# Optimization experiments

Measured on AMD Instinct MI355X. Metric: run time of the kernel, lower is better.

The kernel has to match this reference:

```python
import jax, jax.numpy as jnp
import numpy as np

NUM_HEADS = 16
DIM_HEAD = 64
SCALE = DIM_HEAD ** -0.5
ROPE_BASE = 10000.0


def _rope(t):
    # t: [b, h, n, d] -> rotary embedding with rotate-half convention
    n, d = t.shape[2], t.shape[3]
    inv_freq = 1.0 / (ROPE_BASE ** (jnp.arange(0, d, 2, dtype=jnp.float32) / d))
    freqs = jnp.arange(n, dtype=jnp.float32)[:, None] * inv_freq[None, :]  # [n, d/2]
    cos = jnp.concatenate([jnp.cos(freqs), jnp.cos(freqs)], axis=-1)  # [n, d]
    sin = jnp.concatenate([jnp.sin(freqs), jnp.sin(freqs)], axis=-1)
    t1, t2 = jnp.split(t, 2, axis=-1)
    rot = jnp.concatenate([-t2, t1], axis=-1)
    return t * cos + rot * sin


def setup_inputs() -> dict:
    key = jax.random.key(0)
    k1, k2, k3 = jax.random.split(key, 3)
    B, N, D = 2, 2049, 1024  # 2048 patches + 1 cls token
    x = jax.random.normal(k1, (B, N, D), dtype=jnp.float32)
    ln_gamma = jnp.ones((D,), dtype=jnp.float32)
    ln_beta = jnp.zeros((D,), dtype=jnp.float32)
    w_qkv = jax.random.normal(k2, (D, 3 * NUM_HEADS * DIM_HEAD), dtype=jnp.float32) * 0.02
    w_out = jax.random.normal(k3, (NUM_HEADS * DIM_HEAD, D), dtype=jnp.float32) * 0.02
    return {"x": x, "ln_gamma": ln_gamma, "ln_beta": ln_beta, "w_qkv": w_qkv, "w_out": w_out}


def reference(x, ln_gamma, ln_beta, w_qkv, w_out):
    B, N, D = x.shape
    # LayerNorm (eps=1e-5, torch default)
    mu = jnp.mean(x, axis=-1, keepdims=True)
    var = jnp.mean(jnp.square(x - mu), axis=-1, keepdims=True)
    xn = (x - mu) * jax.lax.rsqrt(var + 1e-5) * ln_gamma + ln_beta
    # QKV projection (no bias)
    qkv = xn @ w_qkv  # [B, N, 3*H*Dh]
    q, k, v = jnp.split(qkv, 3, axis=-1)
    def to_heads(t):
        return t.reshape(B, N, NUM_HEADS, DIM_HEAD).transpose(0, 2, 1, 3)  # [B,H,N,Dh]
    q, k, v = to_heads(q), to_heads(k), to_heads(v)
    # cls token excluded from RoPE
    q = jnp.concatenate([q[:, :, :1, :], _rope(q[:, :, 1:, :])], axis=2)
    k = jnp.concatenate([k[:, :, :1, :], _rope(k[:, :, 1:, :])], axis=2)
    dots = jnp.einsum('bhqd,bhkd->bhqk', q, k) * SCALE
    attn = jax.nn.softmax(dots, axis=-1)
    out = jnp.einsum('bhqk,bhkd->bhqd', attn, v)
    out = out.transpose(0, 2, 1, 3).reshape(B, N, NUM_HEADS * DIM_HEAD)
    return out @ w_out
```

## Files before the change

kernel.cpp:

```cpp
#include <hip/hip_runtime.h>

#define B_    2
#define N_    2049
#define NPAD  2112
#define D_    1024
#define H_    16
#define DH    64
#define MROWS (B_ * N_)
#define MPAD  4224
#define QSCALE 0.18033688011117674f

using bf16x8 = __attribute__((ext_vector_type(8))) short;
using f32x4  = __attribute__((ext_vector_type(4))) float;
using f32x16 = __attribute__((ext_vector_type(16))) float;

#define AS1 __attribute__((address_space(1)))
#define AS3 __attribute__((address_space(3)))

__device__ __forceinline__ float bf2f(short s) {
  union { unsigned u; float f; } a; a.u = ((unsigned)(unsigned short)s) << 16; return a.f;
}
__device__ __forceinline__ short f2bf(float f) {
  union { float f; unsigned u; } a; a.f = f;
  unsigned r = a.u + 0x7fffu + ((a.u >> 16) & 1u);
  return (short)(r >> 16);
}
__device__ __forceinline__ unsigned pack_trunc(float lo, float hi) {
  union { float f; unsigned u; } a, b; a.f = lo; b.f = hi;
  return (b.u & 0xffff0000u) | (a.u >> 16);
}
__device__ __forceinline__ float hexp2(float x) { return __builtin_amdgcn_exp2f(x); }
__device__ __forceinline__ void dma16(const short* g, AS3 short* l) {
  __builtin_amdgcn_global_load_lds((const AS1 unsigned*)g, (AS3 unsigned*)l, 16, 0, 0);
}

__global__ __launch_bounds__(256) void ln_kernel(const float* __restrict__ x,
                                                 const float* __restrict__ gamma,
                                                 const float* __restrict__ beta,
                                                 short* __restrict__ xn) {
  int row = blockIdx.x;
  int tid = threadIdx.x;
  const float4 v = ((const float4*)(x + (size_t)row * D_))[tid];
  float s  = v.x + v.y + v.z + v.w;
  float ss = v.x * v.x + v.y * v.y + v.z * v.z + v.w * v.w;
  for (int o = 1; o < 64; o <<= 1) { s += __shfl_xor(s, o, 64); ss += __shfl_xor(ss, o, 64); }
  __shared__ float sb[4], s2b[4];
  int wid = tid >> 6;
  if ((tid & 63) == 0) { sb[wid] = s; s2b[wid] = ss; }
  __syncthreads();
  float st  = sb[0] + sb[1] + sb[2] + sb[3];
  float sst = s2b[0] + s2b[1] + s2b[2] + s2b[3];
  float mu  = st * (1.0f / D_);
  float var = sst * (1.0f / D_) - mu * mu;
  float rs  = rsqrtf(var + 1e-5f);
  const float4 g  = ((const float4*)gamma)[tid];
  const float4 be = ((const float4*)beta)[tid];
  short4 o4;
  o4.x = f2bf((v.x - mu) * rs * g.x + be.x);
  o4.y = f2bf((v.y - mu) * rs * g.y + be.y);
  o4.z = f2bf((v.z - mu) * rs * g.z + be.z);
  o4.w = f2bf((v.w - mu) * rs * g.w + be.w);
  ((short4*)(xn + (size_t)row * D_))[tid] = o4;
}

__global__ __launch_bounds__(256) void transpose_tiled(const float* __restrict__ in,
                                                       short* __restrict__ out,
                                                       int K, int Nn) {
  __shared__ float T[64][65];
  int k0 = blockIdx.x * 64;
  int n0 = blockIdx.y * 64;
  int t = threadIdx.x;
  int r = t >> 2, c0 = (t & 3) * 16;
  const float* ip = in + (size_t)(k0 + r) * Nn + n0 + c0;
  #pragma unroll
  for (int j = 0; j < 4; ++j) {
    float4 v = *(const float4*)(ip + j * 4);
    T[r][c0 + j * 4 + 0] = v.x; T[r][c0 + j * 4 + 1] = v.y;
    T[r][c0 + j * 4 + 2] = v.z; T[r][c0 + j * 4 + 3] = v.w;
  }
  __syncthreads();
  bf16x8 w0, w1;
  #pragma unroll
  for (int j = 0; j < 8; ++j) {
    w0[j] = f2bf(T[c0 + j][r]);
    w1[j] = f2bf(T[c0 + 8 + j][r]);
  }
  short* op = out + (size_t)(n0 + r) * K + k0 + c0;
  *(bf16x8*)op = w0;
  *(bf16x8*)(op + 8) = w1;
}

#define BM 128
#define BK 32
template <typename OutT>
__global__ __launch_bounds__(256) void gemm128(const short* __restrict__ A,
                                               const short* __restrict__ BT,
                                               OutT* __restrict__ C,
                                               int Mstore, int Ncols, int K) {
  int lane = threadIdx.x & 63, wid = threadIdx.x >> 6;
  int quad = lane >> 4, l16 = lane & 15;
  int wr = wid >> 1, wc = wid & 1;
  int m0 = blockIdx.x * BM;
  int n0 = blockIdx.y * BM;

  __shared__ __align__(16) short Abuf[2][BM * BK];
  __shared__ __align__(16) short Bbuf[2][BM * BK];
  AS3 short* AbufL = (AS3 short*)&Abuf[0][0];
  AS3 short* BbufL = (AS3 short*)&Bbuf[0][0];

  f32x4 acc[4][4] = {};

  int lrow = lane >> 2, lcol8 = (lane & 3) * 8;
  const short* Ag = A  + (size_t)(m0 + lrow) * K + lcol8;
  const short* Bg = BT + (size_t)(n0 + lrow) * K + lcol8;

  auto stage = [&](int kt, int bb) {
    int k0 = kt * BK;
    #pragma unroll
    for (int i = 0; i < 2; ++i) {
      int j = wid * 2 + i;
      dma16(Ag + (size_t)j * 16 * K + k0, AbufL + bb * (BM * BK) + j * 512);
      dma16(Bg + (size_t)j * 16 * K + k0, BbufL + bb * (BM * BK) + j * 512);
    }
  };

  stage(0, 0);
  __syncthreads();

  int KT = K / BK;
  for (int kt = 0; kt < KT; ++kt) {
    int cur = kt & 1;
    if (kt + 1 < KT) stage(kt + 1, cur ^ 1);
    const short* Ab = &Abuf[cur][0];
    const short* Bb = &Bbuf[cur][0];
    bf16x8 af[4], bfr[4];
    #pragma unroll
    for (int s = 0; s < 4; ++s)
      af[s] = *(const bf16x8*)&Ab[(wr * 64 + s * 16 + l16) * BK + quad * 8];
    #pragma unroll
    for (int t = 0; t < 4; ++t)
      bfr[t] = *(const bf16x8*)&Bb[(wc * 64 + t * 16 + l16) * BK + quad * 8];
    #pragma unroll
    for (int s = 0; s < 4; ++s)
      #pragma unroll
      for (int t = 0; t < 4; ++t)
        acc[s][t] = __builtin_amdgcn_mfma_f32_16x16x32_bf16(af[s], bfr[t], acc[s][t], 0, 0, 0);
    __syncthreads();
  }

  #pragma unroll
  for (int s = 0; s < 4; ++s)
    #pragma unroll
    for (int r = 0; r < 4; ++r) {
      int row = m0 + wr * 64 + s * 16 + quad * 4 + r;
      if (row < Mstore) {
        size_t rb = (size_t)row * Ncols + n0 + wc * 64;
        #pragma unroll
        for (int t = 0; t < 4; ++t) {
          float val = acc[s][t][r];
          if constexpr (sizeof(OutT) == 2)
            C[rb + t * 16 + l16] = (OutT)(unsigned short)f2bf(val);
          else
            C[rb + t * 16 + l16] = (OutT)val;
        }
      }
    }
}

__global__ __launch_bounds__(256) void rope_kernel(const short* __restrict__ qkv,
                                                   short* __restrict__ qg,
                                                   short* __restrict__ kfrag,
                                                   short* __restrict__ vfrag) {
  int bh = blockIdx.y;
  int n0 = blockIdx.x * 64;
  int b = bh >> 4, h = bh & 15;
  int t = threadIdx.x;
  int nl = t >> 2;
  int p  = t & 3;
  int n  = n0 + nl;
  size_t hb = (size_t)bh * NPAD * DH;
  size_t ob = hb + (size_t)n * DH;

  __shared__ short Vt[64][66];
  __shared__ short Kt[64][66];

  bf16x8 oq1 = {}, oq2 = {}, ok1 = {}, ok2 = {};
  short v1s[8] = {}, v2s[8] = {};
  if (n < N_) {
    size_t ib = ((size_t)(b * N_ + n)) * 3072 + h * DH;
    bf16x8 q1v = *(const bf16x8*)(qkv + ib + p * 8);
    bf16x8 q2v = *(const bf16x8*)(qkv + ib + 32 + p * 8);
    bf16x8 k1v = *(const bf16x8*)(qkv + ib + 1024 + p * 8);
    bf16x8 k2v = *(const bf16x8*)(qkv + ib + 1024 + 32 + p * 8);
    bf16x8 v1v = *(const bf16x8*)(qkv + ib + 2048 + p * 8);
    bf16x8 v2v = *(const bf16x8*)(qkv + ib + 2048 + 32 + p * 8);
    #pragma unroll
    for (int j = 0; j < 8; ++j) {
      int i = p * 8 + j;
      float q1 = bf2f(q1v[j]), q2 = bf2f(q2v[j]);
      float k1 = bf2f(k1v[j]), k2 = bf2f(k2v[j]);
      if (n > 0) {
        float ang = (float)(n - 1) * powf(10000.0f, -(float)i * (1.0f / 32.0f));
        float sn, cs; sincosf(ang, &sn, &cs);
        float nq1 = q1 * cs - q2 * sn, nq2 = q2 * cs + q1 * sn;
        float nk1 = k1 * cs - k2 * sn, nk2 = k2 * cs + k1 * sn;
        q1 = nq1; q2 = nq2; k1 = nk1; k2 = nk2;
      }
      oq1[j] = f2bf(q1 * QSCALE); oq2[j] = f2bf(q2 * QSCALE);
      ok1[j] = f2bf(k1); ok2[j] = f2bf(k2);
      v1s[j] = v1v[j]; v2s[j] = v2v[j];
    }
  }
  *(bf16x8*)(qg + ob + p * 8)      = oq1;
  *(bf16x8*)(qg + ob + 32 + p * 8) = oq2;
  #pragma unroll
  for (int j = 0; j < 8; ++j) {
    Vt[nl][p * 8 + j]      = v1s[j];
    Vt[nl][32 + p * 8 + j] = v2s[j];
    Kt[nl][p * 8 + j]      = ok1[j];
    Kt[nl][32 + p * 8 + j] = ok2[j];
  }
  __syncthreads();

  int l = t & 63, c = t >> 6;
  int lk = l & 31, hi = l >> 5;
  size_t tb = hb + (size_t)(n0 >> 6) * 4096;
  bf16x8 wv0, wv1, wk0, wk1;
  #pragma unroll
  for (int i = 0; i < 8; ++i) {
    int keyr = c * 16 + hi * 8 + i;
    wv0[i] = Vt[keyr][lk];
    wv1[i] = Vt[keyr][32 + lk];
    wk0[i] = Kt[lk][keyr];
    wk1[i] = Kt[32 + lk][keyr];
  }
  *(bf16x8*)(vfrag + tb + (size_t)(0 * 4 + c) * 512 + l * 8) = wv0;
  *(bf16x8*)(vfrag + tb + (size_t)(4 + c) * 512 + l * 8)     = wv1;
  *(bf16x8*)(kfrag + tb + (size_t)(0 * 4 + c) * 512 + l * 8) = wk0;
  *(bf16x8*)(kfrag + tb + (size_t)(4 + c) * 512 + l * 8)     = wk1;
}

__global__ __launch_bounds__(256, 3) void attn_kernel(const short* __restrict__ qg,
                                                      const short* __restrict__ kfrag,
                                                      const short* __restrict__ vfrag,
                                                      short* __restrict__ Opart,
                                                      float* __restrict__ lpart) {
  int blk = blockIdx.x;
  int xcd = blk & 7;
  int t_  = blk >> 3;
  int bh  = xcd * 4 + (t_ & 3);
  int u   = t_ >> 2;
  int ks  = (u >= 17) ? 1 : 0;
  int qblk = u - ks * 17;
  int kt0 = ks * 17, kt1 = ks ? 32 : 16;

  int lane = threadIdx.x & 63, wid = threadIdx.x >> 6;
  int q    = lane & 31;
  int half = lane >> 5;
  int q0   = qblk * 128 + wid * 32;
  size_t hb = (size_t)bh * NPAD * DH;
  const short* kf_hb = kfrag + hb;
  const short* vf_hb = vfrag + hb;

  __shared__ __align__(16) short Kbuf[3][8 * 512];
  AS3 short* KbufL = (AS3 short*)&Kbuf[0][0];
  const short* KbufR = &Kbuf[0][0];

  int qr = q0 + q; if (qr >= NPAD) qr = 0;
  const short* qp = qg + hb + (size_t)qr * DH + half * 8;
  bf16x8 qf[4];
  #pragma unroll
  for (int s = 0; s < 4; ++s) qf[s] = *(const bf16x8*)(qp + s * 16);

  f32x16 o0 = {}, o1 = {};
  float lrun = 0.0f;

  auto stage = [&](int kt, int bb) {
    const short* src = kf_hb + (size_t)kt * 4096;
    #pragma unroll
    for (int i = 0; i < 2; ++i) {
      int j = wid * 2 + i;
      dma16(src + j * 512 + lane * 8, KbufL + bb * 4096 + j * 512);
    }
  };

  stage(kt0, 0);
  stage(kt0 + 1, 1);

  for (int kt = kt0; kt <= kt1; ++kt) {
    int rb = (kt - kt0) % 3;
    int k0 = kt * 64;

    asm volatile("s_waitcnt vmcnt(2)" ::: "memory");
    __builtin_amdgcn_s_barrier();

    const short* vt = vf_hb + (size_t)kt * 4096;
    bf16x8 vf0[4], vf1[4];
    #pragma unroll
    for (int s = 0; s < 4; ++s) {
      vf0[s] = *(const bf16x8*)(vt + (0 * 4 + s) * 512 + lane * 8);
      vf1[s] = *(const bf16x8*)(vt + (4 + s) * 512 + lane * 8);
    }
    __builtin_amdgcn_sched_barrier(0);
    if (kt + 2 <= kt1) stage(kt + 2, (kt - kt0 + 2) % 3);
    __builtin_amdgcn_sched_barrier(0);

    const short* Kc = KbufR + rb * 4096;
    f32x16 sA = {}, sB = {};
    __builtin_amdgcn_s_setprio(1);
    #pragma unroll
    for (int s = 0; s < 4; ++s) {
      bf16x8 kf0 = *(const bf16x8*)&Kc[(0 * 4 + s) * 512 + lane * 8];
      bf16x8 kf1 = *(const bf16x8*)&Kc[(1 * 4 + s) * 512 + lane * 8];
      sA = __builtin_amdgcn_mfma_f32_32x32x16_bf16(kf0, qf[s], sA, 0, 0, 0);
      sB = __builtin_amdgcn_mfma_f32_32x32x16_bf16(kf1, qf[s], sB, 0, 0, 0);
    }
    __builtin_amdgcn_s_setprio(0);

    if (k0 + 64 > N_) {
      #pragma unroll
      for (int rr = 0; rr < 16; ++rr) {
        int key = (rr & 3) + 8 * (rr >> 2) + 4 * half;
        if (k0 + key >= N_)      sA[rr] = -1e30f;
        if (k0 + 32 + key >= N_) sB[rr] = -1e30f;
      }
    }

    float vsum = 0.0f;
    #pragma unroll
    for (int rr = 0; rr < 16; ++rr) {
      sA[rr] = hexp2(sA[rr]); vsum += sA[rr];
      sB[rr] = hexp2(sB[rr]); vsum += sB[rr];
    }
    lrun += vsum;

    unsigned w[4][4];
    #pragma unroll
    for (int g = 0; g < 2; ++g) {
      #pragma unroll
      for (int fs = 0; fs < 2; ++fs) {
        int b0 = fs * 8;
        float e0, e1, e2, e3, e4, e5, e6, e7;
        if (g == 0) {
          e0 = sA[b0+0]; e1 = sA[b0+1]; e2 = sA[b0+2]; e3 = sA[b0+3];
          e4 = sA[b0+4]; e5 = sA[b0+5]; e6 = sA[b0+6]; e7 = sA[b0+7];
        } else {
          e0 = sB[b0+0]; e1 = sB[b0+1]; e2 = sB[b0+2]; e3 = sB[b0+3];
          e4 = sB[b0+4]; e5 = sB[b0+5]; e6 = sB[b0+6]; e7 = sB[b0+7];
        }
        unsigned X1 = pack_trunc(e0, e1);
        unsigned X2 = pack_trunc(e2, e3);
        unsigned Y1 = pack_trunc(e4, e5);
        unsigned Y2 = pack_trunc(e6, e7);
        asm("v_permlane32_swap_b32 %0, %1" : "+v"(X1), "+v"(Y1));
        asm("v_permlane32_swap_b32 %0, %1" : "+v"(X2), "+v"(Y2));
        int kst = g * 2 + fs;
        w[kst][0] = X1; w[kst][1] = X2; w[kst][2] = Y1; w[kst][3] = Y2;
      }
    }

    __builtin_amdgcn_s_setprio(1);
    #pragma unroll
    for (int kst = 0; kst < 4; ++kst) {
      union { unsigned u[4]; bf16x8 v; } bw;
      bw.u[0] = w[kst][0]; bw.u[1] = w[kst][1]; bw.u[2] = w[kst][2]; bw.u[3] = w[kst][3];
      o0 = __builtin_amdgcn_mfma_f32_32x32x16_bf16(vf0[kst], bw.v, o0, 0, 0, 0);
      o1 = __builtin_amdgcn_mfma_f32_32x32x16_bf16(vf1[kst], bw.v, o1, 0, 0, 0);
    }
    __builtin_amdgcn_s_setprio(0);
  }

  lrun += __shfl_xor(lrun, 32, 64);

  int qrow = q0 + q;
  if (qrow < N_) {
    size_t ob = (((size_t)ks * 32 + bh) * NPAD + qrow) * 64;
    #pragma unroll
    for (int m = 0; m < 2; ++m) {
      #pragma unroll
      for (int gq = 0; gq < 4; ++gq) {
        float a0 = m ? o1[gq*4+0] : o0[gq*4+0];
        float a1 = m ? o1[gq*4+1] : o0[gq*4+1];
        float a2 = m ? o1[gq*4+2] : o0[gq*4+2];
        float a3 = m ? o1[gq*4+3] : o0[gq*4+3];
        short4 st;
        st.x = f2bf(a0); st.y = f2bf(a1); st.z = f2bf(a2); st.w = f2bf(a3);
        int dh = m * 32 + gq * 8 + half * 4;
        *(short4*)(Opart + ob + dh) = st;
      }
    }
    if (half == 0) lpart[((size_t)ks * 32 + bh) * NPAD + qrow] = lrun;
  }
}

__global__ __launch_bounds__(256) void combine_kernel(const short* __restrict__ Opart,
                                                      const float* __restrict__ lpart,
                                                      short* __restrict__ attn_out) {
  int idx = blockIdx.x * 256 + threadIdx.x;
  const int total = 32 * N_ * 16;
  if (idx >= total) return;
  int c4 = idx & 15;
  int t = idx >> 4;
  int n = t % N_;
  int bh = t / N_;
  int b = bh >> 4, h = bh & 15;
  const size_t halfO = (size_t)32 * NPAD * 64;
  size_t off = ((size_t)bh * NPAD + n) * 64 + c4 * 4;
  short4 a  = *(const short4*)(Opart + off);
  short4 bb = *(const short4*)(Opart + halfO + off);
  float la = lpart[(size_t)bh * NPAD + n];
  float lb = lpart[(size_t)32 * NPAD + (size_t)bh * NPAD + n];
  float inv = 1.0f / (la + lb);
  short4 st;
  st.x = f2bf((bf2f(a.x) + bf2f(bb.x)) * inv);
  st.y = f2bf((bf2f(a.y) + bf2f(bb.y)) * inv);
  st.z = f2bf((bf2f(a.z) + bf2f(bb.z)) * inv);
  st.w = f2bf((bf2f(a.w) + bf2f(bb.w)) * inv);
  size_t rowb = ((size_t)(b * N_ + n)) * (H_ * DH) + h * DH + c4 * 4;
  *(short4*)(attn_out + rowb) = st;
}

extern "C" void kernel_launch(void* const* d_in, const int* in_sizes, int n_in,
                              void* d_out, int out_size, void* d_ws, size_t ws_size,
                              hipStream_t stream) {
  const float* x     = (const float*)d_in[0];
  const float* gamma = (const float*)d_in[1];
  const float* beta  = (const float*)d_in[2];
  const float* w_qkv = (const float*)d_in[3];
  const float* w_out = (const float*)d_in[4];

  short* wqkvT = (short*)d_ws;
  short* woutT = wqkvT + (size_t)3072 * 1024;
  short* xn    = woutT + (size_t)1024 * 1024;
  short* qkv   = xn    + (size_t)MPAD * 1024;
  short* qg    = qkv   + (size_t)MPAD * 3072;
  short* kfragG = qg    + (size_t)B_ * H_ * NPAD * DH;
  short* vfragG = kfragG + (size_t)B_ * H_ * NPAD * DH;
  short* attn_out = xn;
  short* Opart = qkv;
  float* lpart = (float*)(qkv + (size_t)2 * 32 * NPAD * 64);

  ln_kernel<<<MROWS, 256, 0, stream>>>(x, gamma, beta, xn);
  {
    dim3 g(1024 / 64, 3072 / 64);
    transpose_tiled<<<g, 256, 0, stream>>>(w_qkv, wqkvT, 1024, 3072);
  }
  {
    dim3 g(1024 / 64, 1024 / 64);
    transpose_tiled<<<g, 256, 0, stream>>>(w_out, woutT, 1024, 1024);
  }
  {
    dim3 g(MPAD / 128, 3072 / 128);
    gemm128<unsigned short><<<g, 256, 0, stream>>>(xn, wqkvT, (unsigned short*)qkv, MROWS, 3072, 1024);
  }
  {
    dim3 g(33, 32);
    rope_kernel<<<g, 256, 0, stream>>>(qkv, qg, kfragG, vfragG);
  }
  attn_kernel<<<8 * 4 * 17 * 2, 256, 0, stream>>>(qg, kfragG, vfragG, Opart, lpart);
  combine_kernel<<<(32 * N_ * 16 + 255) / 256, 256, 0, stream>>>(Opart, lpart, attn_out);
  {
    dim3 g(MPAD / 128, 1024 / 128);
    gemm128<float><<<g, 256, 0, stream>>>(attn_out, woutT, (float*)d_out, MROWS, 1024, 1024);
  }
}
```

Measured before the change: 245.6 us.

## Fuse layernorm and weight transposes into one prep kernel; raise attention occupancy bound

Merges the layernorm kernel and the two weight transpose/convert kernels into a single launch, dispatching by block index, to cut launch overhead and let the pieces overlap. Also raises the attention kernel's min-blocks launch bound from 3 to 8, pushing the compiler to use fewer registers for higher occupancy. That risks register spills in the attention inner loop.

```diff
diff --git a/kernel.cpp b/kernel.cpp
--- a/kernel.cpp
+++ b/kernel.cpp
@@ -34,43 +34,51 @@
   __builtin_amdgcn_global_load_lds((const AS1 unsigned*)g, (AS3 unsigned*)l, 16, 0, 0);
 }
 
-__global__ __launch_bounds__(256) void ln_kernel(const float* __restrict__ x,
-                                                 const float* __restrict__ gamma,
-                                                 const float* __restrict__ beta,
-                                                 short* __restrict__ xn) {
-  int row = blockIdx.x;
+__global__ __launch_bounds__(256) void prep_kernel(const float* __restrict__ x,
+                                                   const float* __restrict__ gamma,
+                                                   const float* __restrict__ beta,
+                                                   short* __restrict__ xn,
+                                                   const float* __restrict__ w_qkv,
+                                                   short* __restrict__ wqkvT,
+                                                   const float* __restrict__ w_out,
+                                                   short* __restrict__ woutT) {
+  int blk = blockIdx.x;
   int tid = threadIdx.x;
-  const float4 v = ((const float4*)(x + (size_t)row * D_))[tid];
-  float s  = v.x + v.y + v.z + v.w;
-  float ss = v.x * v.x + v.y * v.y + v.z * v.z + v.w * v.w;
-  for (int o = 1; o < 64; o <<= 1) { s += __shfl_xor(s, o, 64); ss += __shfl_xor(ss, o, 64); }
+  __shared__ float T[64][65];
   __shared__ float sb[4], s2b[4];
-  int wid = tid >> 6;
-  if ((tid & 63) == 0) { sb[wid] = s; s2b[wid] = ss; }
-  __syncthreads();
-  float st  = sb[0] + sb[1] + sb[2] + sb[3];
-  float sst = s2b[0] + s2b[1] + s2b[2] + s2b[3];
-  float mu  = st * (1.0f / D_);
-  float var = sst * (1.0f / D_) - mu * mu;
-  float rs  = rsqrtf(var + 1e-5f);
-  const float4 g  = ((const float4*)gamma)[tid];
-  const float4 be = ((const float4*)beta)[tid];
-  short4 o4;
-  o4.x = f2bf((v.x - mu) * rs * g.x + be.x);
-  o4.y = f2bf((v.y - mu) * rs * g.y + be.y);
-  o4.z = f2bf((v.z - mu) * rs * g.z + be.z);
-  o4.w = f2bf((v.w - mu) * rs * g.w + be.w);
-  ((short4*)(xn + (size_t)row * D_))[tid] = o4;
-}
-
-__global__ __launch_bounds__(256) void transpose_tiled(const float* __restrict__ in,
-                                                       short* __restrict__ out,
-                                                       int K, int Nn) {
-  __shared__ float T[64][65];
-  int k0 = blockIdx.x * 64;
-  int n0 = blockIdx.y * 64;
-  int t = threadIdx.x;
-  int r = t >> 2, c0 = (t & 3) * 16;
+
+  if (blk < MROWS) {
+    int row = blk;
+    const float4 v = ((const float4*)(x + (size_t)row * D_))[tid];
+    float s  = v.x + v.y + v.z + v.w;
+    float ss = v.x * v.x + v.y * v.y + v.z * v.z + v.w * v.w;
+    for (int o = 1; o < 64; o <<= 1) { s += __shfl_xor(s, o, 64); ss += __shfl_xor(ss, o, 64); }
+    int wid = tid >> 6;
+    if ((tid & 63) == 0) { sb[wid] = s; s2b[wid] = ss; }
+    __syncthreads();
+    float st  = sb[0] + sb[1] + sb[2] + sb[3];
+    float sst = s2b[0] + s2b[1] + s2b[2] + s2b[3];
+    float mu  = st * (1.0f / D_);
+    float var = sst * (1.0f / D_) - mu * mu;
+    float rs  = rsqrtf(var + 1e-5f);
+    const float4 g  = ((const float4*)gamma)[tid];
+    const float4 be = ((const float4*)beta)[tid];
+    short4 o4;
+    o4.x = f2bf((v.x - mu) * rs * g.x + be.x);
+    o4.y = f2bf((v.y - mu) * rs * g.y + be.y);
+    o4.z = f2bf((v.z - mu) * rs * g.z + be.z);
+    o4.w = f2bf((v.w - mu) * rs * g.w + be.w);
+    ((short4*)(xn + (size_t)row * D_))[tid] = o4;
+    return;
+  }
+
+  const float* in; short* out; int K, Nn, t2;
+  int b2 = blk - MROWS;
+  if (b2 < 768) { in = w_qkv; out = wqkvT; K = 1024; Nn = 3072; t2 = b2; }
+  else          { in = w_out; out = woutT; K = 1024; Nn = 1024; t2 = b2 - 768; }
+  int k0 = (t2 & 15) * 64;
+  int n0 = (t2 >> 4) * 64;
+  int r = tid >> 2, c0 = (tid & 3) * 16;
   const float* ip = in + (size_t)(k0 + r) * Nn + n0 + c0;
   #pragma unroll
   for (int j = 0; j < 4; ++j) {
@@ -240,7 +248,7 @@
   *(bf16x8*)(kfrag + tb + (size_t)(4 + c) * 512 + l * 8)     = wk1;
 }
 
-__global__ __launch_bounds__(256, 3) void attn_kernel(const short* __restrict__ qg,
+__global__ __launch_bounds__(256, 8) void attn_kernel(const short* __restrict__ qg,
                                                       const short* __restrict__ kfrag,
                                                       const short* __restrict__ vfrag,
                                                       short* __restrict__ Opart,
@@ -440,15 +448,8 @@
   short* Opart = qkv;
   float* lpart = (float*)(qkv + (size_t)2 * 32 * NPAD * 64);
 
-  ln_kernel<<<MROWS, 256, 0, stream>>>(x, gamma, beta, xn);
-  {
-    dim3 g(1024 / 64, 3072 / 64);
-    transpose_tiled<<<g, 256, 0, stream>>>(w_qkv, wqkvT, 1024, 3072);
-  }
-  {
-    dim3 g(1024 / 64, 1024 / 64);
-    transpose_tiled<<<g, 256, 0, stream>>>(w_out, woutT, 1024, 1024);
-  }
+  prep_kernel<<<MROWS + 768 + 256, 256, 0, stream>>>(x, gamma, beta, xn,
+                                                     w_qkv, wqkvT, w_out, woutT);
   {
     dim3 g(MPAD / 128, 3072 / 128);
     gemm128<unsigned short><<<g, 256, 0, stream>>>(xn, wqkvT, (unsigned short*)qkv, MROWS, 3072, 1024);
```

After: 254.0 us. +3.4%, slower.
